# Optimization experiments

Measured on AMD Instinct MI355X. Metric: run time of the kernel, lower is better.

Reference implementation:

```python
import jax, jax.numpy as jnp
import numpy as np

N = 8192      # num nodes (pad index == N, matching the original's 15004 sentinel)
IN = 128; H = 128; OUT = 128
T = 512       # number of teams
L = 30        # max_len
SAMPLE = 5    # sample team size
DCAT = 2 * H + OUT


def _glorot(k, shape):
    lim = np.sqrt(6.0 / (shape[0] + shape[1]))
    return jax.random.uniform(k, shape, jnp.float32, -lim, lim)


def setup_inputs() -> dict:
    key = jax.random.key(0)
    ks = jax.random.split(key, 32)
    x = jax.random.normal(ks[0], (1, N, IN), jnp.float32)
    # sparse-ish binary dense adjacency, avg degree ~16 (memory-bound adj@x)
    adj = (jax.random.uniform(ks[1], (1, N, N), jnp.float32) < 16.0 / N).astype(jnp.float32)
    # team index matrix, ragged lengths in [SAMPLE+1, L], padded with N
    lens = jax.random.randint(ks[2], (T,), SAMPLE + 1, L + 1)
    ids = jax.random.randint(ks[3], (T, L), 0, N)
    teams = jnp.where(jnp.arange(L)[None, :] < lens[:, None], ids, N)
    # DenseGraphConv params: lin_rel (W,b) on adj@x, lin_root (no bias) on x
    p = dict(
        W1r=_glorot(ks[4], (IN, H)), b1=jnp.zeros((H,), jnp.float32), W1s=_glorot(ks[5], (IN, H)),
        W2r=_glorot(ks[6], (H, H)), b2=jnp.zeros((H,), jnp.float32), W2s=_glorot(ks[7], (H, H)),
        W3r=_glorot(ks[8], (H, OUT)), b3=jnp.zeros((OUT,), jnp.float32), W3s=_glorot(ks[9], (H, OUT)),
        g1=jnp.ones((H,), jnp.float32), be1=jnp.zeros((H,), jnp.float32),
        g2=jnp.ones((H,), jnp.float32), be2=jnp.zeros((H,), jnp.float32),
        g3=jnp.ones((OUT,), jnp.float32), be3=jnp.zeros((OUT,), jnp.float32),
        Wl=_glorot(ks[10], (DCAT, OUT)), bl=jnp.zeros((OUT,), jnp.float32),
        att=_glorot(ks[11], (T, L)),  # xavier_uniform'd attention vectors
    )
    return dict(x=x, adj=adj, teams=teams, sample_len=SAMPLE, **p)


def _bn(h, g, b):
    # BatchNorm1d in training mode over flattened (B*N, C), biased variance
    B, n, C = h.shape
    h2 = h.reshape(-1, C)
    mu = h2.mean(0)
    var = h2.var(0)
    return (((h2 - mu) * jax.lax.rsqrt(var + 1e-5)) * g + b).reshape(B, n, C)


def _conv(x, adj, Wr, br, Ws):
    # DenseGraphConv: lin_rel(adj @ x) + lin_root(x)
    return jnp.einsum('bnm,bmf,fo->bno', adj, x, Wr) + br + jnp.einsum('bnf,fo->bno', x, Ws)


def reference(x, adj, teams, sample_len, W1r, b1, W1s, W2r, b2, W2s, W3r, b3, W3s,
              g1, be1, g2, be2, g3, be3, Wl, bl, att):
    x1 = _bn(jax.nn.relu(_conv(x, adj, W1r, b1, W1s)), g1, be1)
    x2 = _bn(jax.nn.relu(_conv(x1, adj, W2r, b2, W2s)), g2, be2)
    x3 = _bn(jax.nn.relu(_conv(x2, adj, W3r, b3, W3s)), g3, be3)
    xcat = jnp.concatenate([x1, x2, x3], axis=-1)               # [1,N,DCAT]
    s = jax.nn.relu(xcat @ Wl + bl)
    appended = jnp.concatenate([xcat[0], jnp.zeros((1, xcat.shape[-1]), xcat.dtype)], 0)  # [N+1,D]
    gathered = appended[teams]                                   # [T,L,D] ragged gather
    # team: full softmax over attention vector (pad positions keep softmax mass,
    # but gather the zero row -> contribute zero, matching the original)
    a_team = jax.nn.softmax(att, axis=-1)
    team_emb = jnp.einsum('tl,tld->td', a_team, gathered)
    pos = jnp.arange(teams.shape[1])[None, :]
    # sample: sub-softmax over the attention entries at the sample members' positions
    m_s = pos < sample_len
    a_s = jax.nn.softmax(jnp.where(m_s, att, -1e30), axis=-1)
    sample_emb = jnp.einsum('tl,tld->td', a_s, gathered)
    # remain: team minus sample minus pad sentinel
    m_r = (pos >= sample_len) & (teams != N)
    a_r = jax.nn.softmax(jnp.where(m_r, att, -1e30), axis=-1)
    remain_emb = jnp.einsum('tl,tld->td', a_r, gathered)
    return s, xcat, team_emb, sample_emb, remain_emb
```

## Files before the change

kernel.cpp:

```cpp
#include <hip/hip_runtime.h>
#include <stdint.h>

#define NN 8192
#define CC 128
#define TT 512
#define LL 30
#define CAP 64

typedef unsigned int uint32;
typedef unsigned short u16;

typedef float f32x4 __attribute__((ext_vector_type(4)));
typedef short bf16x8 __attribute__((ext_vector_type(8)));

__device__ __forceinline__ float bf2f(uint32 h) { return __uint_as_float(h << 16); }
__device__ __forceinline__ u16 f2bf(float f) {
    uint32 u = __float_as_uint(f);
    u = (u + 0x7fffu + ((u >> 16) & 1u)) >> 16;
    return (u16)u;
}
__device__ __forceinline__ uint32 pack2(float a, float b) {
    return (uint32)f2bf(a) | ((uint32)f2bf(b) << 16);
}

__device__ __forceinline__ void stats_reduce(const float* __restrict__ P,
                                             const float* __restrict__ g,
                                             const float* __restrict__ be,
                                             float* __restrict__ coefOut, int tid) {
    __shared__ float SS[256], QQ[256];
    int c = tid & 127, half = tid >> 7;
    float s = 0.f, q = 0.f;
    int b0 = half * 128;
#pragma unroll 8
    for (int b = b0; b < b0 + 128; ++b) {
        s += P[b * 256 + c];
        q += P[b * 256 + 128 + c];
    }
    SS[tid] = s; QQ[tid] = q;
    __syncthreads();
    if (tid < 128) {
        float sum = SS[tid] + SS[tid + 128];
        float sq = QQ[tid] + QQ[tid + 128];
        float mu = sum * (1.f / NN);
        float var = sq * (1.f / NN) - mu * mu;
        float rs = rsqrtf(var + 1e-5f);
        float a = g[tid] * rs;
        coefOut[tid] = a;
        coefOut[128 + tid] = be[tid] - mu * a;
    }
}

__global__ __launch_bounds__(256) void k_pre(
    const float* __restrict__ adj,
    const float* __restrict__ W1r, const float* __restrict__ W1s,
    const float* __restrict__ W2r, const float* __restrict__ W2s,
    const float* __restrict__ W3r, const float* __restrict__ W3s,
    const float* __restrict__ Wl, const float* __restrict__ x0,
    int* __restrict__ nbr, int* __restrict__ cnt,
    u16* __restrict__ wfrag, u16* __restrict__ x0bf,
    u16* __restrict__ yp1, u16* __restrict__ yp2, u16* __restrict__ yp3,
    float* __restrict__ coefs) {
    int b = blockIdx.x, tid = threadIdx.x;
    if (b < 2048) {
        int row = b * 4 + (tid >> 6);
        int lane = tid & 63;
        const float4* arow = (const float4*)(adj + (size_t)row * NN);
        int base = 0;
        int* dst = nbr + (size_t)row * CAP;
        for (int it = 0; it < 32; ++it) {
            float4 v = arow[it * 64 + lane];
            float vv[4] = {v.x, v.y, v.z, v.w};
#pragma unroll
            for (int j = 0; j < 4; ++j) {
                unsigned long long m = __ballot(vv[j] != 0.f);
                if (vv[j] != 0.f) {
                    int pos = base + __popcll(m & ((1ull << lane) - 1ull));
                    if (pos < CAP) dst[pos] = it * 256 + lane * 4 + j;
                }
                base += __popcll(m);
            }
        }
        int nn = base < CAP ? base : CAP;
        int npad = (nn + 3) & ~3;
        for (int p = nn + lane; p < npad; p += 64) dst[p] = NN;
        if (lane == 0) cnt[row] = nn;
    } else if (b < 2336) {
        int bb = b - 2048;
        const float* Wa;
        const float* Wb;
        int tile, gbase;
        if (bb < 64)       { Wa = W1r; Wb = W1s; tile = bb;       gbase = 0; }
        else if (bb < 128) { Wa = W2r; Wb = W2s; tile = bb - 64;  gbase = 64; }
        else if (bb < 192) { Wa = W3r; Wb = W3s; tile = bb - 128; gbase = 128; }
        else               { Wa = Wl;  Wb = nullptr; tile = bb - 192; gbase = 192; }
        int kt = tile >> 3, nt = tile & 7;
        int lane = tid & 63, i0 = (tid >> 6) * 2;
        int n = nt * 16 + (lane & 15);
        u16* dst = wfrag + ((size_t)(gbase + tile) * 64 + lane) * 8;
#pragma unroll
        for (int ii = 0; ii < 2; ++ii) {
            int i = i0 + ii;
            int k = kt * 32 + ((lane >> 4) * 8) + i;
            float v;
            if (Wb) v = (k < 128) ? Wa[k * CC + n] : Wb[(k - 128) * CC + n];
            else    v = Wa[k * CC + n];
            dst[i] = f2bf(v);
        }
    } else if (b < 3360) {
        int idx = (b - 2336) * 1024 + tid * 4;
        float4 v = *(const float4*)(x0 + idx);
        ushort4 o;
        o.x = f2bf(v.x); o.y = f2bf(v.y); o.z = f2bf(v.z); o.w = f2bf(v.w);
        *(ushort4*)(x0bf + idx) = o;
    } else {
        if (tid < 128) {
            x0bf[(size_t)NN * CC + tid] = 0;
            yp1[(size_t)NN * CC + tid] = 0;
            yp2[(size_t)NN * CC + tid] = 0;
            yp3[(size_t)NN * CC + tid] = 0;
            coefs[tid] = 1.f;
            coefs[128 + tid] = 0.f;
        }
    }
}

__global__ __launch_bounds__(256) void k_agg(const u16* __restrict__ src,
                                             const int* __restrict__ nbr,
                                             const int* __restrict__ cnt,
                                             u16* __restrict__ Abraw,
                                             const float* __restrict__ P,
                                             const float* __restrict__ g,
                                             const float* __restrict__ be,
                                             float* __restrict__ coefOut) {
    if (blockIdx.x >= 2048) {
        stats_reduce(P, g, be, coefOut, threadIdx.x);
        return;
    }
    int row = blockIdx.x * 4 + (threadIdx.x >> 6);
    int lane = threadIdx.x & 63;
    int c = lane * 2;
    int nreal = cnt[row];
    int npad = (nreal + 3) & ~3;
    const int* nb = nbr + (size_t)row * CAP;
    float a0 = 0.f, a1 = 0.f;
    for (int j = 0; j < npad; j += 4) {
        int4 m = *(const int4*)(nb + j);
        uint32 v0 = *(const uint32*)(src + (size_t)m.x * CC + c);
        uint32 v1 = *(const uint32*)(src + (size_t)m.y * CC + c);
        uint32 v2 = *(const uint32*)(src + (size_t)m.z * CC + c);
        uint32 v3 = *(const uint32*)(src + (size_t)m.w * CC + c);
        a0 += bf2f(v0 & 0xffffu); a1 += bf2f(v0 >> 16);
        a0 += bf2f(v1 & 0xffffu); a1 += bf2f(v1 >> 16);
        a0 += bf2f(v2 & 0xffffu); a1 += bf2f(v2 >> 16);
        a0 += bf2f(v3 & 0xffffu); a1 += bf2f(v3 >> 16);
    }
    *(uint32*)(Abraw + (size_t)row * CC + c) = pack2(a0, a1);
}

__global__ __launch_bounds__(512) void k_gemm(const u16* __restrict__ Abraw,
                                              const u16* __restrict__ yprev,
                                              const int* __restrict__ cnt,
                                              const u16* __restrict__ wfrag,
                                              const float* __restrict__ bias,
                                              const float* __restrict__ coefIn,
                                              u16* __restrict__ yp,
                                              float* __restrict__ partials) {
    __shared__ u16 A[32][264];
    __shared__ float sSum[CC], sSq[CC];
    int tid = threadIdx.x, lane = tid & 63, wid = tid >> 6;
    int row0 = blockIdx.x * 32;
    if (tid < CC) { sSum[tid] = 0.f; sSq[tid] = 0.f; }
    for (int i = tid; i < 1024; i += 512) {
        int r = i >> 5, k = (i & 31) * 8;
        int row = row0 + r;
        uint4 raw;
        float fn;
        int c;
        if (k < 128) {
            c = k;
            raw = *(const uint4*)(Abraw + (size_t)row * CC + k);
            fn = (float)cnt[row];
        } else {
            c = k - 128;
            raw = *(const uint4*)(yprev + (size_t)row * CC + c);
            fn = 1.f;
        }
        float4 a0 = *(const float4*)(coefIn + c);
        float4 a1 = *(const float4*)(coefIn + c + 4);
        float4 b0 = *(const float4*)(coefIn + 128 + c);
        float4 b1 = *(const float4*)(coefIn + 128 + c + 4);
        uint4 o;
        o.x = pack2(a0.x * bf2f(raw.x & 0xffffu) + b0.x * fn, a0.y * bf2f(raw.x >> 16) + b0.y * fn);
        o.y = pack2(a0.z * bf2f(raw.y & 0xffffu) + b0.z * fn, a0.w * bf2f(raw.y >> 16) + b0.w * fn);
        o.z = pack2(a1.x * bf2f(raw.z & 0xffffu) + b1.x * fn, a1.y * bf2f(raw.z >> 16) + b1.y * fn);
        o.w = pack2(a1.z * bf2f(raw.w & 0xffffu) + b1.z * fn, a1.w * bf2f(raw.w >> 16) + b1.w * fn);
        *(uint4*)&A[r][k] = o;
    }
    __syncthreads();

    int mh = wid >> 2, nh = wid & 3;
    int arow = mh * 16 + (lane & 15);
    int kg = (lane >> 4) * 8;
    f32x4 acc[2];
#pragma unroll
    for (int nt = 0; nt < 2; ++nt) acc[nt] = (f32x4){0.f, 0.f, 0.f, 0.f};
#pragma unroll
    for (int kt = 0; kt < 8; ++kt) {
        bf16x8 a = *(const bf16x8*)&A[arow][kt * 32 + kg];
        const u16* wb = wfrag + ((size_t)(kt * 8 + nh * 2) * 64 + lane) * 8;
#pragma unroll
        for (int nt = 0; nt < 2; ++nt) {
            bf16x8 bfr = *(const bf16x8*)(wb + (size_t)nt * 512);
            acc[nt] = __builtin_amdgcn_mfma_f32_16x16x32_bf16(a, bfr, acc[nt], 0, 0, 0);
        }
    }
    int rowb = row0 + mh * 16 + ((lane >> 4) * 4);
#pragma unroll
    for (int nt = 0; nt < 2; ++nt) {
        int col = nh * 32 + nt * 16 + (lane & 15);
        float bv = bias[col];
        float s1 = 0.f, s2 = 0.f;
#pragma unroll
        for (int q = 0; q < 4; ++q) {
            float y = acc[nt][q] + bv;
            y = y > 0.f ? y : 0.f;
            yp[(size_t)(rowb + q) * CC + col] = f2bf(y);
            s1 += y;
            s2 += y * y;
        }
        s1 += __shfl_xor(s1, 16); s1 += __shfl_xor(s1, 32);
        s2 += __shfl_xor(s2, 16); s2 += __shfl_xor(s2, 32);
        if ((lane >> 4) == 0) { atomicAdd(&sSum[col], s1); atomicAdd(&sSq[col], s2); }
    }
    __syncthreads();
    if (tid < CC) {
        partials[(size_t)blockIdx.x * 256 + tid] = sSum[tid];
        partials[(size_t)blockIdx.x * 256 + CC + tid] = sSq[tid];
    }
}

__global__ __launch_bounds__(256) void k_coef3(const float* __restrict__ P,
                                               const float* __restrict__ g,
                                               const float* __restrict__ be,
                                               float* __restrict__ coefOut) {
    stats_reduce(P, g, be, coefOut, threadIdx.x);
}

__global__ __launch_bounds__(256) void k_out(
    const u16* __restrict__ yp1, const u16* __restrict__ yp2, const u16* __restrict__ yp3,
    const float* __restrict__ coefs,
    const u16* __restrict__ wfrag, const float* __restrict__ bias,
    const int* __restrict__ teams, const int* __restrict__ slen_p,
    const float* __restrict__ att,
    float* __restrict__ sout, float* __restrict__ xcat,
    float* __restrict__ oT, float* __restrict__ oS, float* __restrict__ oR) {
    int b = blockIdx.x, tid = threadIdx.x;
    if (b < 512) {
        __shared__ u16 A[16][392];
        int lane = tid & 63, wid = tid >> 6;
        int row0 = b * 16;
        for (int i = tid; i < 768; i += 256) {
            int r = i / 48, kk = (i % 48) * 8;
            int seg = kk >> 7, c = kk & 127;
            const u16* sp = (seg == 0 ? yp1 : seg == 1 ? yp2 : yp3) + (size_t)(row0 + r) * CC + c;
            uint4 raw = *(const uint4*)sp;
            const float* cf = coefs + seg * 256;
            float4 av0 = *(const float4*)(cf + c);
            float4 av1 = *(const float4*)(cf + c + 4);
            float4 bv0 = *(const float4*)(cf + 128 + c);
            float4 bv1 = *(const float4*)(cf + 128 + c + 4);
            uint4 o;
            o.x = pack2(av0.x * bf2f(raw.x & 0xffffu) + bv0.x, av0.y * bf2f(raw.x >> 16) + bv0.y);
            o.y = pack2(av0.z * bf2f(raw.y & 0xffffu) + bv0.z, av0.w * bf2f(raw.y >> 16) + bv0.w);
            o.z = pack2(av1.x * bf2f(raw.z & 0xffffu) + bv1.x, av1.y * bf2f(raw.z >> 16) + bv1.y);
            o.w = pack2(av1.z * bf2f(raw.w & 0xffffu) + bv1.z, av1.w * bf2f(raw.w >> 16) + bv1.w);
            *(uint4*)&A[r][kk] = o;
        }
        __syncthreads();
        int nh = wid;
        int arow = lane & 15;
        int kg = (lane >> 4) * 8;
        f32x4 acc[2];
#pragma unroll
        for (int nt = 0; nt < 2; ++nt) acc[nt] = (f32x4){0.f, 0.f, 0.f, 0.f};
#pragma unroll
        for (int kt = 0; kt < 12; ++kt) {
            bf16x8 a = *(const bf16x8*)&A[arow][kt * 32 + kg];
            const u16* wb = wfrag + ((size_t)(kt * 8 + nh * 2) * 64 + lane) * 8;
#pragma unroll
            for (int nt = 0; nt < 2; ++nt) {
                bf16x8 bfr = *(const bf16x8*)(wb + (size_t)nt * 512);
                acc[nt] = __builtin_amdgcn_mfma_f32_16x16x32_bf16(a, bfr, acc[nt], 0, 0, 0);
            }
        }
        int rowb = row0 + ((lane >> 4) * 4);
#pragma unroll
        for (int nt = 0; nt < 2; ++nt) {
            int col = nh * 32 + nt * 16 + (lane & 15);
            float bv = bias[col];
#pragma unroll
            for (int q = 0; q < 4; ++q) {
                float y = acc[nt][q] + bv;
                sout[(size_t)(rowb + q) * CC + col] = y > 0.f ? y : 0.f;
            }
        }
    } else if (b < 1024) {
        __shared__ float wT[LL], wS[LL], wR[LL];
        __shared__ int ids[LL];
        int t = b - 512;
        if (tid < 64) {
            int lane = tid;
            bool act = lane < LL;
            float a = act ? att[t * LL + lane] : 0.f;
            int id = act ? teams[t * LL + lane] : NN;
            if (act) ids[lane] = id;
            int sl = *slen_p;
            const float NEG = -1e30f;
            float v = act ? a : NEG;
#pragma unroll
            for (int o = 32; o > 0; o >>= 1) v = fmaxf(v, __shfl_xor(v, o));
            float mT = v;
            float eT = act ? __expf(a - mT) : 0.f;
            v = eT;
#pragma unroll
            for (int o = 32; o > 0; o >>= 1) v += __shfl_xor(v, o);
            float sT = v;
            bool inS = act && (lane < sl);
            v = inS ? a : NEG;
#pragma unroll
            for (int o = 32; o > 0; o >>= 1) v = fmaxf(v, __shfl_xor(v, o));
            float mS = v;
            float eS = inS ? __expf(a - mS) : 0.f;
            v = eS;
#pragma unroll
            for (int o = 32; o > 0; o >>= 1) v += __shfl_xor(v, o);
            float sS = v;
            bool inR = act && (lane >= sl) && (id != NN);
            v = inR ? a : NEG;
#pragma unroll
            for (int o = 32; o > 0; o >>= 1) v = fmaxf(v, __shfl_xor(v, o));
            float mR = v;
            float eR = inR ? __expf(a - mR) : 0.f;
            v = eR;
#pragma unroll
            for (int o = 32; o > 0; o >>= 1) v += __shfl_xor(v, o);
            float sR = v;
            if (act) {
                wT[lane] = eT / sT;
                wS[lane] = eS / sS;
                wR[lane] = eR / sR;
            }
        }
        __syncthreads();
        for (int d = tid; d < 384; d += 256) {
            int seg = d >> 7, c = d & 127;
            const u16* xb = seg == 0 ? yp1 : seg == 1 ? yp2 : yp3;
            float ca = coefs[seg * 256 + c];
            float cb = coefs[seg * 256 + 128 + c];
            float aT = 0.f, aS = 0.f, aR = 0.f;
            for (int l = 0; l < LL; ++l) {
                int id = ids[l];
                if (id < NN) {
                    float vv = ca * bf2f((uint32)xb[(size_t)id * CC + c]) + cb;
                    aT += wT[l] * vv;
                    aS += wS[l] * vv;
                    aR += wR[l] * vv;
                }
            }
            oT[(size_t)t * 384 + d] = aT;
            oS[(size_t)t * 384 + d] = aS;
            oR[(size_t)t * 384 + d] = aR;
        }
    } else {
        int idx = (b - 1024) * 256 + tid;
        int n = idx / 96;
        int k = (idx % 96) * 4;
        int seg = k >> 7, c = k & 127;
        const u16* sp = (seg == 0 ? yp1 : seg == 1 ? yp2 : yp3) + (size_t)n * CC + c;
        ushort4 raw = *(const ushort4*)sp;
        const float* cf = coefs + seg * 256;
        float4 a = *(const float4*)(cf + c);
        float4 bb = *(const float4*)(cf + 128 + c);
        float4 o;
        o.x = a.x * bf2f((uint32)raw.x) + bb.x;
        o.y = a.y * bf2f((uint32)raw.y) + bb.y;
        o.z = a.z * bf2f((uint32)raw.z) + bb.z;
        o.w = a.w * bf2f((uint32)raw.w) + bb.w;
        *(float4*)(xcat + (size_t)n * 384 + k) = o;
    }
}

extern "C" void kernel_launch(void* const* d_in, const int* in_sizes, int n_in,
                              void* d_out, int out_size, void* d_ws, size_t ws_size,
                              hipStream_t stream) {
    const float* x = (const float*)d_in[0];
    const float* adj = (const float*)d_in[1];
    const int* teams = (const int*)d_in[2];
    const int* slen = (const int*)d_in[3];
    const float* W1r = (const float*)d_in[4];
    const float* b1 = (const float*)d_in[5];
    const float* W1s = (const float*)d_in[6];
    const float* W2r = (const float*)d_in[7];
    const float* b2 = (const float*)d_in[8];
    const float* W2s = (const float*)d_in[9];
    const float* W3r = (const float*)d_in[10];
    const float* b3 = (const float*)d_in[11];
    const float* W3s = (const float*)d_in[12];
    const float* g1 = (const float*)d_in[13];
    const float* be1 = (const float*)d_in[14];
    const float* g2 = (const float*)d_in[15];
    const float* be2 = (const float*)d_in[16];
    const float* g3 = (const float*)d_in[17];
    const float* be3 = (const float*)d_in[18];
    const float* Wl = (const float*)d_in[19];
    const float* bl = (const float*)d_in[20];
    const float* att = (const float*)d_in[21];

    float* out = (float*)d_out;
    float* s_out = out;
    float* xcat = out + (size_t)NN * CC;
    float* oT = xcat + (size_t)NN * 384;
    float* oS = oT + (size_t)TT * 384;
    float* oR = oS + (size_t)TT * 384;

    char* ws = (char*)d_ws;
    size_t off = 0;
    int* nbr = (int*)(ws + off); off += (size_t)NN * CAP * 4;
    int* cnt = (int*)(ws + off); off += (size_t)NN * 4;
    u16* x0bf = (u16*)(ws + off); off += (size_t)(NN + 1) * CC * 2;
    u16* yp1 = (u16*)(ws + off); off += (size_t)(NN + 1) * CC * 2;
    u16* yp2 = (u16*)(ws + off); off += (size_t)(NN + 1) * CC * 2;
    u16* yp3 = (u16*)(ws + off); off += (size_t)(NN + 1) * CC * 2;
    u16* Abraw = (u16*)(ws + off); off += (size_t)NN * CC * 2;
    u16* wfrag = (u16*)(ws + off); off += (size_t)288 * 512 * 2;
    float* partials = (float*)(ws + off); off += (size_t)256 * 256 * 4;
    float* coefs = (float*)(ws + off); off += (size_t)4 * 256 * 4;

    k_pre<<<3361, 256, 0, stream>>>(adj, W1r, W1s, W2r, W2s, W3r, W3s, Wl, x,
                                    nbr, cnt, wfrag, x0bf, yp1, yp2, yp3, coefs);
    k_agg<<<2048, 256, 0, stream>>>(x0bf, nbr, cnt, Abraw, partials, g1, be1, coefs + 256);
    k_gemm<<<256, 512, 0, stream>>>(Abraw, x0bf, cnt, wfrag, b1, coefs, yp1, partials);
    k_agg<<<2049, 256, 0, stream>>>(yp1, nbr, cnt, Abraw, partials, g1, be1, coefs + 256);
    k_gemm<<<256, 512, 0, stream>>>(Abraw, yp1, cnt, wfrag + 64 * 512, b2, coefs + 256, yp2, partials);
    k_agg<<<2049, 256, 0, stream>>>(yp2, nbr, cnt, Abraw, partials, g2, be2, coefs + 512);
    k_gemm<<<256, 512, 0, stream>>>(Abraw, yp2, cnt, wfrag + 128 * 512, b3, coefs + 512, yp3, partials);
    k_coef3<<<1, 256, 0, stream>>>(partials, g3, be3, coefs + 768);
    k_out<<<4096, 256, 0, stream>>>(yp1, yp2, yp3, coefs + 256,
                                    wfrag + 192 * 512, bl, teams, slen, att,
                                    s_out, xcat, oT, oS, oR);
}
```

Before: 128.4 us.

## Fuse first-layer aggregation into adjacency scan and halve GEMM row tile

The first-layer neighbour aggregation over x0 is now done inside k_pre, right after each row's neighbour list is built, so the first k_agg launch is removed. The GEMM kernel now handles 16 rows per block instead of 32, with each wave owning one 16-column tile, and the grid doubles to 512 blocks. The BN partials buffer and stats reduction loop are resized to 512 entries to match. This saves a launch and a pass over the neighbour lists and gives the GEMM more parallelism, in exchange for more partials to reduce. It also reads fp32 x0 directly in the fused loop, and it leaves a duplicated o.w assignment whose first instance is overwritten.

New measurement: 144.9 us. +12.8%, slower.

```diff
diff --git a/kernel.cpp b/kernel.cpp
--- a/kernel.cpp
+++ b/kernel.cpp
@@ -30,9 +30,9 @@
     __shared__ float SS[256], QQ[256];
     int c = tid & 127, half = tid >> 7;
     float s = 0.f, q = 0.f;
-    int b0 = half * 128;
+    int b0 = half * 256;
 #pragma unroll 8
-    for (int b = b0; b < b0 + 128; ++b) {
+    for (int b = b0; b < b0 + 256; ++b) {
         s += P[b * 256 + c];
         q += P[b * 256 + 128 + c];
     }
@@ -59,7 +59,7 @@
     int* __restrict__ nbr, int* __restrict__ cnt,
     u16* __restrict__ wfrag, u16* __restrict__ x0bf,
     u16* __restrict__ yp1, u16* __restrict__ yp2, u16* __restrict__ yp3,
-    float* __restrict__ coefs) {
+    u16* __restrict__ Abraw, float* __restrict__ coefs) {
     int b = blockIdx.x, tid = threadIdx.x;
     if (b < 2048) {
         int row = b * 4 + (tid >> 6);
@@ -84,6 +84,16 @@
         int npad = (nn + 3) & ~3;
         for (int p = nn + lane; p < npad; p += 64) dst[p] = NN;
         if (lane == 0) cnt[row] = nn;
+        int c = lane * 2;
+        float a0 = 0.f, a1 = 0.f;
+        for (int j = 0; j < npad; j += 4) {
+            int4 m = *(const int4*)(dst + j);
+            if (m.x < NN) { float2 v = *(const float2*)(x0 + (size_t)m.x * CC + c); a0 += v.x; a1 += v.y; }
+            if (m.y < NN) { float2 v = *(const float2*)(x0 + (size_t)m.y * CC + c); a0 += v.x; a1 += v.y; }
+            if (m.z < NN) { float2 v = *(const float2*)(x0 + (size_t)m.z * CC + c); a0 += v.x; a1 += v.y; }
+            if (m.w < NN) { float2 v = *(const float2*)(x0 + (size_t)m.w * CC + c); a0 += v.x; a1 += v.y; }
+        }
+        *(uint32*)(Abraw + (size_t)row * CC + c) = pack2(a0, a1);
     } else if (b < 2336) {
         int bb = b - 2048;
         const float* Wa;
@@ -165,13 +175,12 @@
                                               const float* __restrict__ coefIn,
                                               u16* __restrict__ yp,
                                               float* __restrict__ partials) {
-    __shared__ u16 A[32][264];
+    __shared__ u16 A[16][264];
     __shared__ float sSum[CC], sSq[CC];
     int tid = threadIdx.x, lane = tid & 63, wid = tid >> 6;
-    int row0 = blockIdx.x * 32;
-    if (tid < CC) { sSum[tid] = 0.f; sSq[tid] = 0.f; }
-    for (int i = tid; i < 1024; i += 512) {
-        int r = i >> 5, k = (i & 31) * 8;
+    int row0 = blockIdx.x * 16;
+    {
+        int r = tid >> 5, k = (tid & 31) * 8;
         int row = row0 + r;
         uint4 raw;
         float fn;
@@ -193,50 +202,39 @@
         o.x = pack2(a0.x * bf2f(raw.x & 0xffffu) + b0.x * fn, a0.y * bf2f(raw.x >> 16) + b0.y * fn);
         o.y = pack2(a0.z * bf2f(raw.y & 0xffffu) + b0.z * fn, a0.w * bf2f(raw.y >> 16) + b0.w * fn);
         o.z = pack2(a1.x * bf2f(raw.z & 0xffffu) + b1.x * fn, a1.y * bf2f(raw.z >> 16) + b1.y * fn);
+        o.w = pack2(a1.z * bf2f(raw.w & 0xffffu) + b1.w * fn, a1.w * bf2f(raw.w >> 16) + b1.w * fn);
         o.w = pack2(a1.z * bf2f(raw.w & 0xffffu) + b1.z * fn, a1.w * bf2f(raw.w >> 16) + b1.w * fn);
         *(uint4*)&A[r][k] = o;
     }
     __syncthreads();
 
-    int mh = wid >> 2, nh = wid & 3;
-    int arow = mh * 16 + (lane & 15);
+    int arow = lane & 15;
     int kg = (lane >> 4) * 8;
-    f32x4 acc[2];
-#pragma unroll
-    for (int nt = 0; nt < 2; ++nt) acc[nt] = (f32x4){0.f, 0.f, 0.f, 0.f};
+    f32x4 acc = (f32x4){0.f, 0.f, 0.f, 0.f};
 #pragma unroll
     for (int kt = 0; kt < 8; ++kt) {
         bf16x8 a = *(const bf16x8*)&A[arow][kt * 32 + kg];
-        const u16* wb = wfrag + ((size_t)(kt * 8 + nh * 2) * 64 + lane) * 8;
-#pragma unroll
-        for (int nt = 0; nt < 2; ++nt) {
-            bf16x8 bfr = *(const bf16x8*)(wb + (size_t)nt * 512);
-            acc[nt] = __builtin_amdgcn_mfma_f32_16x16x32_bf16(a, bfr, acc[nt], 0, 0, 0);
-        }
-    }
-    int rowb = row0 + mh * 16 + ((lane >> 4) * 4);
-#pragma unroll
-    for (int nt = 0; nt < 2; ++nt) {
-        int col = nh * 32 + nt * 16 + (lane & 15);
-        float bv = bias[col];
-        float s1 = 0.f, s2 = 0.f;
-#pragma unroll
-        for (int q = 0; q < 4; ++q) {
-            float y = acc[nt][q] + bv;
-            y = y > 0.f ? y : 0.f;
-            yp[(size_t)(rowb + q) * CC + col] = f2bf(y);
-            s1 += y;
-            s2 += y * y;
-        }
-        s1 += __shfl_xor(s1, 16); s1 += __shfl_xor(s1, 32);
-        s2 += __shfl_xor(s2, 16); s2 += __shfl_xor(s2, 32);
-        if ((lane >> 4) == 0) { atomicAdd(&sSum[col], s1); atomicAdd(&sSq[col], s2); }
-    }
+        bf16x8 bfr = *(const bf16x8*)(wfrag + ((size_t)(kt * 8 + wid) * 64 + lane) * 8);
+        acc = __builtin_amdgcn_mfma_f32_16x16x32_bf16(a, bfr, acc, 0, 0, 0);
+    }
+    int rowb = row0 + ((lane >> 4) * 4);
+    int col = wid * 16 + (lane & 15);
+    float bv = bias[col];
+    float s1 = 0.f, s2 = 0.f;
+#pragma unroll
+    for (int q = 0; q < 4; ++q) {
+        float y = acc[q] + bv;
+        y = y > 0.f ? y : 0.f;
+        yp[(size_t)(rowb + q) * CC + col] = f2bf(y);
+        s1 += y;
+        s2 += y * y;
+    }
+    s1 += __shfl_xor(s1, 16); s1 += __shfl_xor(s1, 32);
+    s2 += __shfl_xor(s2, 16); s2 += __shfl_xor(s2, 32);
+    if (lane < 16) { sSum[col] = s1; sSq[col] = s2; }
     __syncthreads();
-    if (tid < CC) {
-        partials[(size_t)blockIdx.x * 256 + tid] = sSum[tid];
-        partials[(size_t)blockIdx.x * 256 + CC + tid] = sSq[tid];
-    }
+    if (tid < 128) partials[(size_t)blockIdx.x * 256 + tid] = sSum[tid];
+    else if (tid < 256) partials[(size_t)blockIdx.x * 256 + tid] = sSq[tid - 128];
 }
 
 __global__ __launch_bounds__(256) void k_coef3(const float* __restrict__ P,
@@ -433,17 +431,16 @@
     u16* yp3 = (u16*)(ws + off); off += (size_t)(NN + 1) * CC * 2;
     u16* Abraw = (u16*)(ws + off); off += (size_t)NN * CC * 2;
     u16* wfrag = (u16*)(ws + off); off += (size_t)288 * 512 * 2;
-    float* partials = (float*)(ws + off); off += (size_t)256 * 256 * 4;
+    float* partials = (float*)(ws + off); off += (size_t)512 * 256 * 4;
     float* coefs = (float*)(ws + off); off += (size_t)4 * 256 * 4;
 
     k_pre<<<3361, 256, 0, stream>>>(adj, W1r, W1s, W2r, W2s, W3r, W3s, Wl, x,
-                                    nbr, cnt, wfrag, x0bf, yp1, yp2, yp3, coefs);
-    k_agg<<<2048, 256, 0, stream>>>(x0bf, nbr, cnt, Abraw, partials, g1, be1, coefs + 256);
-    k_gemm<<<256, 512, 0, stream>>>(Abraw, x0bf, cnt, wfrag, b1, coefs, yp1, partials);
+                                    nbr, cnt, wfrag, x0bf, yp1, yp2, yp3, Abraw, coefs);
+    k_gemm<<<512, 512, 0, stream>>>(Abraw, x0bf, cnt, wfrag, b1, coefs, yp1, partials);
     k_agg<<<2049, 256, 0, stream>>>(yp1, nbr, cnt, Abraw, partials, g1, be1, coefs + 256);
-    k_gemm<<<256, 512, 0, stream>>>(Abraw, yp1, cnt, wfrag + 64 * 512, b2, coefs + 256, yp2, partials);
+    k_gemm<<<512, 512, 0, stream>>>(Abraw, yp1, cnt, wfrag + 64 * 512, b2, coefs + 256, yp2, partials);
     k_agg<<<2049, 256, 0, stream>>>(yp2, nbr, cnt, Abraw, partials, g2, be2, coefs + 512);
-    k_gemm<<<256, 512, 0, stream>>>(Abraw, yp2, cnt, wfrag + 128 * 512, b3, coefs + 512, yp3, partials);
+    k_gemm<<<512, 512, 0, stream>>>(Abraw, yp2, cnt, wfrag + 128 * 512, b3, coefs + 512, yp3, partials);
     k_coef3<<<1, 256, 0, stream>>>(partials, g3, be3, coefs + 768);
     k_out<<<4096, 256, 0, stream>>>(yp1, yp2, yp3, coefs + 256,
                                     wfrag + 192 * 512, bl, teams, slen, att,
```
